# Optimization experiments

Hardware: AMD Instinct MI355X
Metric: run time of the kernel (lower is better)

## Reference

```python
import jax, jax.numpy as jnp
import numpy as np

# Hyperparameters (DetectionLoss __init__ defaults)
ALPHA = 0.75
GAMMA = 2.0
NUM_NEG = 10000
NUM_HARD = 100
NEG_POS_RATIO = 100
FN_WEIGHT = 4.0
FN_THRESHOLD = 0.8
HFP_T1 = 0.5
HFP_T2 = 0.7
HFP_W1 = 1.5
HFP_W2 = 2.0

B, N = 16, 884736  # batch, num anchor points (96^3 crop)


def setup_inputs() -> dict:
    key = jax.random.key(0)
    kp, kt, km = jax.random.split(key, 3)
    pred = jax.random.normal(kp, (B, N, 1), dtype=jnp.float32)
    # sparse binary positive targets (~440 positives per sample)
    target = (jax.random.uniform(kt, (B, N, 1)) < 5e-4).astype(jnp.float32)
    mask_ignore = (jax.random.uniform(km, (B, N, 1)) < 1e-2).astype(jnp.float32)
    mask_ignore = mask_ignore * (1.0 - target)
    return {"pred": pred, "target": target, "mask_ignore": mask_ignore}


def _bce_with_logits(x, t):
    # numerically stable binary_cross_entropy_with_logits, reduction='none'
    return jnp.maximum(x, 0.0) - x * t + jnp.log1p(jnp.exp(-jnp.abs(x)))


def _cls_loss(pred, target, mask_ignore):
    b = pred.shape[0]
    pred = pred.reshape(b, -1)
    target = target.reshape(b, -1)
    mask_ignore = mask_ignore.reshape(b, -1)
    # fixed keys replace python random.sample for negative subsampling
    keys = jax.random.split(jax.random.key(42), b)

    def per_sample(pred_b, target_b, mask_b, key):
        is_pos = target_b == 1.0
        is_neg = target_b == 0.0
        cls_prob = jnp.clip(jax.nn.sigmoid(jax.lax.stop_gradient(pred_b)), 1e-4, 1.0 - 1e-4)
        alpha_factor = jnp.where(is_pos, ALPHA, 1.0 - ALPHA)
        focal_w = alpha_factor * jnp.where(is_pos, 1.0 - cls_prob, cls_prob) ** GAMMA
        loss = jnp.where(mask_b == 0.0, focal_w * _bce_with_logits(pred_b, target_b), 0.0)
        npos = jnp.sum(is_pos)
        # false-negative upweight (only positive points qualify, so it is a
        # no-op in the npos==0 branch, matching the torch control flow)
        loss = loss * jnp.where((cls_prob < FN_THRESHOLD) & is_pos, FN_WEIGHT, 1.0)
        # hard false-positive upweight (applied in both branches)
        hfp_w = HFP_W1 + jnp.clip((cls_prob - HFP_T1) / (HFP_T2 - HFP_T1), 0.0, 1.0) * (HFP_W2 - HFP_W1)
        loss = loss * jnp.where((cls_prob > HFP_T1) & is_neg, hfp_w, 1.0)
        pos_loss = jnp.sum(jnp.where(is_pos, loss, 0.0))
        # random subsample of NUM_NEG negatives without replacement:
        # top-NUM_NEG by uniform random score restricted to negatives
        rnd = jax.random.uniform(key, pred_b.shape)
        sample_score = jnp.where(is_neg, rnd, -jnp.inf)
        _, idx = jax.lax.top_k(sample_score, NUM_NEG)
        neg_losses = jnp.where(is_neg[idx], loss[idx], 0.0)
        # hard-negative mining: keep top-k of the sampled negative losses
        topv = jax.lax.top_k(neg_losses, NUM_NEG)[0]
        k = jnp.where(npos > 0, jnp.minimum(NEG_POS_RATIO * npos, NUM_NEG), NUM_HARD)
        neg_sum = jnp.sum(jnp.where(jnp.arange(NUM_NEG) < k, topv, 0.0))
        # pos branch divides both sums by npos; neg branch divides by 1
        denom = jnp.where(npos > 0, jnp.maximum(npos.astype(pred_b.dtype), 1.0), 1.0)
        return pos_loss / denom, neg_sum / denom

    pos, neg = jax.vmap(per_sample)(pred, target, mask_ignore, keys)
    cls_pos_loss = jnp.sum(pos) / b
    cls_neg_loss = jnp.sum(neg) / b
    return jnp.stack([cls_pos_loss, cls_neg_loss])


def reference(pred, target, mask_ignore):
    return _cls_loss(pred, target, mask_ignore)
```

## Files before the change

### kernel.cpp

```cpp
#include <hip/hip_runtime.h>
#include <stdint.h>


#define BATCH 16
#define NPTS 884736u
#define THRESH_KEY 8266976u
#define THRESH_W   4232691712u
#define KEYMAX 8388607u
#define KSEL 10000u
#define TLO 8285746u
#define THI 8301746u
#define TLO_W 4242301952u
#define HI_W  4250494464u
#define WCAP 3072u
#define LCAP 64
#define SCAP 160
#define BCAP 64
#define NBLK 432u
#define EPT 8u
#define HDRB 512


struct KeyPairs { unsigned k[2 * BATCH]; };

__host__ __device__ __forceinline__ void tf2x32(unsigned k0, unsigned k1,
                                                unsigned x0, unsigned x1,
                                                unsigned& o0, unsigned& o1)
{
  unsigned ks0 = k0, ks1 = k1, ks2 = k0 ^ k1 ^ 0x1BD11BDAu;
  x0 += ks0; x1 += ks1;
#define TF_R(r) { x0 += x1; x1 = __builtin_rotateleft32(x1, r); x1 ^= x0; }
  TF_R(13) TF_R(15) TF_R(26) TF_R(6)
  x0 += ks1; x1 += ks2 + 1u;
  TF_R(17) TF_R(29) TF_R(16) TF_R(24)
  x0 += ks2; x1 += ks0 + 2u;
  TF_R(13) TF_R(15) TF_R(26) TF_R(6)
  x0 += ks0; x1 += ks1 + 3u;
  TF_R(17) TF_R(29) TF_R(16) TF_R(24)
  x0 += ks1; x1 += ks2 + 4u;
  TF_R(13) TF_R(15) TF_R(26) TF_R(6)
  x0 += ks2; x1 += ks0 + 5u;
#undef TF_R
  o0 = x0; o1 = x1;
}

__device__ __forceinline__ float lossf(float x, float t, float m)
{
  float e  = __expf(-x);
  float p  = __fdividef(1.0f, 1.0f + e);
  p = fminf(fmaxf(p, 1e-4f), 1.0f - 1e-4f);
  bool is_pos = (t == 1.0f);
  float alpha = is_pos ? 0.75f : 0.25f;
  float pw = is_pos ? (1.0f - p) : p;
  float soft = __logf(1.0f + __expf(-fabsf(x)));
  float bce = fmaxf(x, 0.0f) - x * t + soft;
  float L = (m == 0.0f) ? alpha * pw * pw * bce : 0.0f;
  if (is_pos && p < 0.8f) L *= 4.0f;
  if (!is_pos && p > 0.5f)
    L *= 1.5f + fminf(fmaxf((p - 0.5f) * 5.0f, 0.0f), 1.0f) * 0.5f;
  return L;
}

__global__ __launch_bounds__(256) void mono(
    const float* __restrict__ pred, const float* __restrict__ target,
    const float* __restrict__ mask, char* __restrict__ hdr,
    unsigned* __restrict__ wkey, unsigned* __restrict__ widx,
    float* __restrict__ wloss, KeyPairs kp)
{
  const int b = blockIdx.y;
  const int tid = threadIdx.x;
  const unsigned i0 = (blockIdx.x * 256u + tid) * EPT;
  const size_t sbase = (size_t)b * NPTS;
  const size_t off = sbase + i0;
  const unsigned k0 = kp.k[2 * b], k1 = kp.k[2 * b + 1];
  char* line = hdr + (size_t)b * HDRB;

  __shared__ unsigned s_n, s_wn, s_base, s_candhi, s_pos;
  __shared__ float    s_psum, s_hsum;
  __shared__ unsigned s_si[SCAP], s_skey[SCAP];
  __shared__ unsigned s_wk[LCAP], s_wi[LCAP];
  __shared__ float    s_wl[LCAP];

  if (tid == 0) {
    s_n = 0; s_wn = 0; s_candhi = 0; s_pos = 0;
    s_psum = 0.0f; s_hsum = 0.0f;
  }
  __syncthreads();

  float4 t4a = *reinterpret_cast<const float4*>(target + off);
  float4 t4b = *reinterpret_cast<const float4*>(target + off + 4);
  float tv[8] = { t4a.x, t4a.y, t4a.z, t4a.w, t4b.x, t4b.y, t4b.z, t4b.w };

  unsigned kw[8];
#pragma unroll
  for (int r = 0; r < 8; ++r) {
    unsigned o0, o1;
    tf2x32(k0, k1, 0u, i0 + (unsigned)r, o0, o1);
    kw[r] = o0 ^ o1;
  }

  unsigned candm = 0, posm = 0, him = 0, winm = 0;
#pragma unroll
  for (int r = 0; r < 8; ++r) {
    bool c  = (tv[r] == 0.0f) && (kw[r] >= THRESH_W);
    bool hi = c && (kw[r] >= HI_W);
    bool wn = c && !hi && (kw[r] >= TLO_W);
    candm |= (unsigned)c  << r;
    him   |= (unsigned)hi << r;
    winm  |= (unsigned)wn << r;
    posm  |= (unsigned)(tv[r] == 1.0f) << r;
  }

  if (candm) atomicAdd(&s_candhi, (unsigned)__popc(candm) | ((unsigned)__popc(him) << 16));
  if (posm)  atomicAdd(&s_pos, (unsigned)__popc(posm));

  const unsigned flags = him | winm | posm;
  if (flags) {
#pragma unroll
    for (int r = 0; r < 8; ++r) {
      if ((flags >> r) & 1u) {
        unsigned cls = ((posm >> r) & 1u) ? 2u : (((winm >> r) & 1u) ? 1u : 0u);
        unsigned p = atomicAdd(&s_n, 1u);
        if (p < SCAP) {
          s_si[p] = (i0 + (unsigned)r) | (cls << 20);
          s_skey[p] = kw[r] >> 9;
        } else {
          float x = pred[off + r], m = mask[off + r];
          float L = lossf(x, (cls == 2u) ? 1.0f : 0.0f, m);
          if (cls == 2u) atomicAdd(&s_psum, L);
          else if (cls == 0u) atomicAdd(&s_hsum, L);
          else {
            unsigned w = atomicAdd(&s_wn, 1u);
            if (w < LCAP) { s_wk[w] = kw[r] >> 9; s_wi[w] = i0 + (unsigned)r; s_wl[w] = L; }
          }
        }
      }
    }
  }
  __syncthreads();

  unsigned n = s_n < SCAP ? s_n : SCAP;
  for (unsigned e = tid; e < n; e += 256) {
    unsigned rec = s_si[e];
    unsigned i = rec & 0xFFFFFu, cls = rec >> 20;
    float x = pred[sbase + i], m = mask[sbase + i];
    float L = lossf(x, (cls == 2u) ? 1.0f : 0.0f, m);
    if (cls == 2u) atomicAdd(&s_psum, L);
    else if (cls == 0u) atomicAdd(&s_hsum, L);
    else {
      unsigned w = atomicAdd(&s_wn, 1u);
      if (w < LCAP) { s_wk[w] = s_skey[e]; s_wi[w] = i; s_wl[w] = L; }
    }
  }
  __syncthreads();

  if (tid == 0) {
    unsigned c = s_candhi & 0xFFFFu, h = s_candhi >> 16, p = s_pos;
    if (c) atomicAdd((unsigned*)(line + 64), c);
    if (h) { atomicAdd((unsigned*)(line + 128), h); atomicAdd((float*)(line + 132), s_hsum); }
    if (p) { atomicAdd((unsigned*)(line + 4), p); atomicAdd((float*)(line + 0), s_psum); }
    unsigned wn = s_wn;
    if (wn > LCAP) { atomicOr((unsigned*)(line + 196), 1u); wn = LCAP; }
    s_base = wn ? atomicAdd((unsigned*)(line + 192), wn) : 0u;
    s_wn = wn;
  }
  __syncthreads();
  unsigned wn = s_wn, gb = s_base;
  for (unsigned e = tid; e < wn; e += 256) {
    unsigned g = gb + e;
    if (g < WCAP) {
      wkey[b * WCAP + g] = s_wk[e];
      widx[b * WCAP + g] = s_wi[e];
      wloss[b * WCAP + g] = s_wl[e];
    }
  }
}

__global__ __launch_bounds__(256) void select_k(
    const float* __restrict__ pred, const float* __restrict__ target,
    const float* __restrict__ mask, char* __restrict__ hdr,
    const unsigned* __restrict__ wkey, const unsigned* __restrict__ widx,
    const float* __restrict__ wloss, float* __restrict__ out, KeyPairs kp)
{
  const int b = blockIdx.x;
  const int tid = threadIdx.x;
  char* line = hdr + (size_t)b * HDRB;
  unsigned* ticket = (unsigned*)(hdr + (size_t)BATCH * HDRB - 4);

  __shared__ unsigned skey[WCAP], sidx[WCAP];
  __shared__ float    sls[WCAP];
  __shared__ unsigned redu[256];
  __shared__ float    redf[256];
  __shared__ unsigned s_eqc, s_u1, s_tick;
  __shared__ unsigned s_eqi[BCAP];
  __shared__ float    s_eql[BCAP];
  __shared__ float    s_f;

  const unsigned cnt    = *(const unsigned*)(line + 64);
  const unsigned n_hi   = *(const unsigned*)(line + 128);
  const float    sum_hi = *(const float*)(line + 132);
  const unsigned n_win  = *(const unsigned*)(line + 192);
  const unsigned fail   = *(const unsigned*)(line + 196);
  const unsigned npos   = *(const unsigned*)(line + 4);
  const bool take_all = (cnt <= KSEL);
  const unsigned nsel = take_all ? cnt : KSEL;
  const unsigned k = (npos > 0u) ? ((100u * npos < KSEL) ? 100u * npos : KSEL) : 100u;
  const bool bad = fail || take_all || (n_hi > KSEL) ||
                   (n_hi + n_win < KSEL) || (n_win > WCAP) || (k < nsel);

  auto redSumU = [&](unsigned v) -> unsigned {
    redu[tid] = v; __syncthreads();
    for (int s = 128; s > 0; s >>= 1) { if (tid < s) redu[tid] += redu[tid + s]; __syncthreads(); }
    unsigned r = redu[0]; __syncthreads(); return r;
  };
  auto redSumF = [&](float v) -> float {
    redf[tid] = v; __syncthreads();
    for (int s = 128; s > 0; s >>= 1) { if (tid < s) redf[tid] += redf[tid + s]; __syncthreads(); }
    float r = redf[0]; __syncthreads(); return r;
  };

  float res = 0.0f;

  if (!bad) {
    const unsigned nw = n_win;
    for (unsigned e = tid; e < nw; e += 256) {
      skey[e] = wkey[b * WCAP + e];
      sidx[e] = widx[b * WCAP + e];
      sls[e]  = wloss[b * WCAP + e];
    }
    __syncthreads();
    const unsigned need = KSEL - n_hi;
    if (need == 0) res = sum_hi;
    else {
      auto cGe = [&](unsigned v) -> unsigned {
        unsigned c = 0;
        for (unsigned e = tid; e < nw; e += 256) c += (skey[e] >= v) ? 1u : 0u;
        return redSumU(c);
      };
      unsigned lo = TLO, hi = THI;
      while (lo < hi) {
        unsigned mid = lo + (hi - lo + 1u) / 2u;
        if (cGe(mid) >= need) lo = mid; else hi = mid - 1u;
      }
      const unsigned V = lo;
      const unsigned c_gt = cGe(V + 1u);
      const unsigned m = need - c_gt;
      float s = 0.0f;
      for (unsigned e = tid; e < nw; e += 256) if (skey[e] > V) s += sls[e];
      float sum_gt = redSumF(s);
      if (tid == 0) s_eqc = 0;
      __syncthreads();
      for (unsigned e = tid; e < nw; e += 256) {
        if (skey[e] == V) {
          unsigned p = atomicAdd(&s_eqc, 1u);
          if (p < BCAP) { s_eqi[p] = sidx[e]; s_eql[p] = sls[e]; }
        }
      }
      __syncthreads();
      if (tid == 0) {
        unsigned ne = s_eqc; if (ne > BCAP) ne = BCAP;
        unsigned mm = (m < ne) ? m : ne;
        float es = 0.0f;
        for (unsigned a = 0; a < mm; ++a) {
          unsigned best = a;
          for (unsigned q = a + 1; q < ne; ++q)
            if (s_eqi[q] < s_eqi[best]) best = q;
          unsigned ti = s_eqi[a]; s_eqi[a] = s_eqi[best]; s_eqi[best] = ti;
          float tl = s_eql[a]; s_eql[a] = s_eql[best]; s_eql[best] = tl;
          es += s_eql[a];
        }
        s_f = sum_hi + sum_gt + es;
      }
      __syncthreads();
      res = s_f;
    }
  } else {
    const float* T = target + (size_t)b * NPTS;
    const float* P = pred   + (size_t)b * NPTS;
    const float* M = mask   + (size_t)b * NPTS;
    const unsigned k0 = kp.k[2 * b], k1 = kp.k[2 * b + 1];
    auto keyOf = [&](unsigned i) -> unsigned {
      unsigned o0, o1; tf2x32(k0, k1, 0u, i, o0, o1); return (o0 ^ o1) >> 9;
    };
    auto cKeyGe = [&](unsigned v) -> unsigned {
      unsigned c = 0;
      for (unsigned i = tid; i < NPTS; i += 256)
        if (T[i] == 0.0f && keyOf(i) >= v) c++;
      return redSumU(c);
    };
    unsigned V = 0, idxcut = 0xffffffffu; float eq_sum = 0.0f;
    if (!take_all) {
      unsigned lo = THRESH_KEY, hi = KEYMAX;
      while (lo < hi) {
        unsigned mid = lo + (hi - lo + 1u) / 2u;
        if (cKeyGe(mid) >= KSEL) lo = mid; else hi = mid - 1u;
      }
      V = lo;
      unsigned c_gt = cKeyGe(V + 1u);
      unsigned needq = KSEL - c_gt;
      if (tid == 0) s_eqc = 0;
      __syncthreads();
      for (unsigned i = tid; i < NPTS; i += 256)
        if (T[i] == 0.0f && keyOf(i) == V) {
          unsigned p = atomicAdd(&s_eqc, 1u);
          if (p < BCAP) s_eqi[p] = i;
        }
      __syncthreads();
      if (tid == 0) {
        unsigned ne = s_eqc; if (ne > BCAP) ne = BCAP;
        unsigned mm = (needq < ne) ? needq : ne;
        float es = 0.0f; unsigned ic = 0xffffffffu;
        for (unsigned a = 0; a < mm; ++a) {
          unsigned best = a;
          for (unsigned q = a + 1; q < ne; ++q)
            if (s_eqi[q] < s_eqi[best]) best = q;
          unsigned ti = s_eqi[a]; s_eqi[a] = s_eqi[best]; s_eqi[best] = ti;
          es += lossf(P[s_eqi[a]], 0.0f, M[s_eqi[a]]);
        }
        if (mm > 0) ic = s_eqi[mm - 1];
        s_f = es; s_u1 = ic;
      }
      __syncthreads();
      eq_sum = s_f; idxcut = s_u1;
      __syncthreads();
    }
    if (k >= nsel) {
      float s = 0.0f;
      for (unsigned i = tid; i < NPTS; i += 256) {
        if (T[i] != 0.0f) continue;
        unsigned kk = keyOf(i);
        if (kk < THRESH_KEY) continue;
        if (take_all || kk > V) s += lossf(P[i], 0.0f, M[i]);
      }
      res = redSumF(s) + (take_all ? 0.0f : eq_sum);
    } else {
      auto cLossGe = [&](unsigned w) -> unsigned {
        unsigned c = 0;
        for (unsigned i = tid; i < NPTS; i += 256) {
          if (T[i] != 0.0f) continue;
          unsigned kk = keyOf(i);
          if (kk < THRESH_KEY) continue;
          bool sel = take_all || kk > V || (kk == V && i <= idxcut);
          if (sel && __float_as_uint(lossf(P[i], 0.0f, M[i])) >= w) c++;
        }
        return redSumU(c);
      };
      unsigned lo = 0u, hi = 0x7f7fffffu;
      while (lo < hi) {
        unsigned mid = lo + (hi - lo + 1u) / 2u;
        if (cLossGe(mid) >= k) lo = mid; else hi = mid - 1u;
      }
      unsigned cgt = cLossGe(lo + 1u);
      float s = 0.0f;
      for (unsigned i = tid; i < NPTS; i += 256) {
        if (T[i] != 0.0f) continue;
        unsigned kk = keyOf(i);
        if (kk < THRESH_KEY) continue;
        bool sel = take_all || kk > V || (kk == V && i <= idxcut);
        float L = lossf(P[i], 0.0f, M[i]);
        if (sel && __float_as_uint(L) > lo) s += L;
      }
      res = redSumF(s) + (float)(k - cgt) * __uint_as_float(lo);
    }
  }

  if (tid == 0) {
    atomicExch((float*)(line + 256), res);
    __threadfence();
    s_tick = atomicAdd(ticket, 1u);
  }
  __syncthreads();
  if (s_tick == BATCH - 1) {
    float ps = 0.0f, ns = 0.0f;
    if (tid < BATCH) {
      char* ln = hdr + (size_t)tid * HDRB;
      float pp = atomicAdd((float*)(ln + 0), 0.0f);
      unsigned np = atomicAdd((unsigned*)(ln + 4), 0u);
      float nr = atomicAdd((float*)(ln + 256), 0.0f);
      float denom = (np > 0u) ? fmaxf((float)np, 1.0f) : 1.0f;
      ps = pp / denom;
      ns = nr / denom;
    }
#pragma unroll
    for (int s = 8; s > 0; s >>= 1) {
      ps += __shfl_down(ps, s, 64);
      ns += __shfl_down(ns, s, 64);
    }
    if (tid == 0) {
      out[0] = ps / (float)BATCH;
      out[1] = ns / (float)BATCH;
    }
  }
}

extern "C" void kernel_launch(void* const* d_in, const int* in_sizes, int n_in,
                              void* d_out, int out_size, void* d_ws, size_t ws_size,
                              hipStream_t stream)
{
  const float* pred   = (const float*)d_in[0];
  const float* target = (const float*)d_in[1];
  const float* mask   = (const float*)d_in[2];
  float* out = (float*)d_out;

  const size_t HDRSZ = (size_t)BATCH * HDRB;
  const size_t FIXED = HDRSZ + 3 * (size_t)BATCH * WCAP * 4;
  if (ws_size < FIXED || out_size < 2) {
    hipMemsetAsync(d_out, 0, sizeof(float) * (out_size > 0 ? out_size : 1), stream);
    return;
  }

  char* ws = (char*)d_ws;
  char*     hdr   = ws;
  unsigned* wkey  = (unsigned*)(ws + HDRSZ);
  unsigned* widx  = wkey + (size_t)BATCH * WCAP;
  float*    wloss = (float*)(widx + (size_t)BATCH * WCAP);

  KeyPairs kp;
  for (unsigned b = 0; b < BATCH; ++b) {
    unsigned o0, o1;
    tf2x32(0u, 42u, 0u, b, o0, o1);
    kp.k[2 * b] = o0; kp.k[2 * b + 1] = o1;
  }

  hipMemsetAsync(hdr, 0, HDRSZ, stream);

  mono<<<dim3(NBLK, BATCH), 256, 0, stream>>>(pred, target, mask, hdr,
                                              wkey, widx, wloss, kp);
  select_k<<<BATCH, 256, 0, stream>>>(pred, target, mask, hdr,
                                      wkey, widx, wloss, out, kp);
}
```

Measured before the change: 85.06 us.

## Fuse selection into the main kernel via a per-sample last-block ticket

The separate select_k launch is removed. Each block of the streaming kernel takes a per-sample atomic ticket after writing its winners, and the last block of each sample runs the threshold selection and final reduction. To keep shared memory low, only keys are staged in LDS and index/loss values are re-read from global memory. This saves a kernel launch and its gap, but raises LDS use for every block of the big grid, which may reduce occupancy of the streaming phase.

```diff
diff --git a/kernel.cpp b/kernel.cpp
--- a/kernel.cpp
+++ b/kernel.cpp
@@ -61,11 +61,11 @@
   return L;
 }
 
-__global__ __launch_bounds__(256) void mono(
+__global__ __launch_bounds__(256) void fused(
     const float* __restrict__ pred, const float* __restrict__ target,
     const float* __restrict__ mask, char* __restrict__ hdr,
     unsigned* __restrict__ wkey, unsigned* __restrict__ widx,
-    float* __restrict__ wloss, KeyPairs kp)
+    float* __restrict__ wloss, float* __restrict__ out, KeyPairs kp)
 {
   const int b = blockIdx.y;
   const int tid = threadIdx.x;
@@ -74,12 +74,22 @@
   const size_t off = sbase + i0;
   const unsigned k0 = kp.k[2 * b], k1 = kp.k[2 * b + 1];
   char* line = hdr + (size_t)b * HDRB;
-
-  __shared__ unsigned s_n, s_wn, s_base, s_candhi, s_pos;
+  unsigned* gticket = (unsigned*)(hdr + (size_t)BATCH * HDRB - 4);
+
+  __shared__ unsigned s_n, s_wn, s_base, s_candhi, s_pos, s_tick;
   __shared__ float    s_psum, s_hsum;
   __shared__ unsigned s_si[SCAP], s_skey[SCAP];
   __shared__ unsigned s_wk[LCAP], s_wi[LCAP];
   __shared__ float    s_wl[LCAP];
+  __shared__ unsigned skey[WCAP];
+  __shared__ unsigned redu[256];
+  __shared__ float    redf[256];
+  __shared__ unsigned s_eqc, s_u1, s_fin;
+  __shared__ unsigned s_eqi[BCAP];
+  __shared__ float    s_eql[BCAP];
+  __shared__ float    s_f;
+  __shared__ unsigned h_cnt, h_nhi, h_nwin, h_fail, h_npos;
+  __shared__ float    h_sumhi;
 
   if (tid == 0) {
     s_n = 0; s_wn = 0; s_candhi = 0; s_pos = 0;
@@ -165,43 +175,37 @@
     s_wn = wn;
   }
   __syncthreads();
-  unsigned wn = s_wn, gb = s_base;
-  for (unsigned e = tid; e < wn; e += 256) {
-    unsigned g = gb + e;
-    if (g < WCAP) {
-      wkey[b * WCAP + g] = s_wk[e];
-      widx[b * WCAP + g] = s_wi[e];
-      wloss[b * WCAP + g] = s_wl[e];
-    }
-  }
-}
-
-__global__ __launch_bounds__(256) void select_k(
-    const float* __restrict__ pred, const float* __restrict__ target,
-    const float* __restrict__ mask, char* __restrict__ hdr,
-    const unsigned* __restrict__ wkey, const unsigned* __restrict__ widx,
-    const float* __restrict__ wloss, float* __restrict__ out, KeyPairs kp)
-{
-  const int b = blockIdx.x;
-  const int tid = threadIdx.x;
-  char* line = hdr + (size_t)b * HDRB;
-  unsigned* ticket = (unsigned*)(hdr + (size_t)BATCH * HDRB - 4);
-
-  __shared__ unsigned skey[WCAP], sidx[WCAP];
-  __shared__ float    sls[WCAP];
-  __shared__ unsigned redu[256];
-  __shared__ float    redf[256];
-  __shared__ unsigned s_eqc, s_u1, s_tick;
-  __shared__ unsigned s_eqi[BCAP];
-  __shared__ float    s_eql[BCAP];
-  __shared__ float    s_f;
-
-  const unsigned cnt    = *(const unsigned*)(line + 64);
-  const unsigned n_hi   = *(const unsigned*)(line + 128);
-  const float    sum_hi = *(const float*)(line + 132);
-  const unsigned n_win  = *(const unsigned*)(line + 192);
-  const unsigned fail   = *(const unsigned*)(line + 196);
-  const unsigned npos   = *(const unsigned*)(line + 4);
+  {
+    unsigned wn = s_wn, gb = s_base;
+    for (unsigned e = tid; e < wn; e += 256) {
+      unsigned g = gb + e;
+      if (g < WCAP) {
+        wkey[b * WCAP + g] = s_wk[e];
+        widx[b * WCAP + g] = s_wi[e];
+        wloss[b * WCAP + g] = s_wl[e];
+      }
+    }
+  }
+
+  if (tid == 0) {
+    __threadfence();
+    s_tick = atomicAdd((unsigned*)(line + 200), 1u);
+  }
+  __syncthreads();
+  if (s_tick != NBLK - 1) return;
+
+  if (tid == 0) {
+    h_cnt   = atomicAdd((unsigned*)(line + 64), 0u);
+    h_nhi   = atomicAdd((unsigned*)(line + 128), 0u);
+    h_sumhi = atomicAdd((float*)(line + 132), 0.0f);
+    h_nwin  = atomicAdd((unsigned*)(line + 192), 0u);
+    h_fail  = atomicAdd((unsigned*)(line + 196), 0u);
+    h_npos  = atomicAdd((unsigned*)(line + 4), 0u);
+  }
+  __syncthreads();
+  const unsigned cnt = h_cnt, n_hi = h_nhi, n_win = h_nwin, fail = h_fail,
+                 npos = h_npos;
+  const float sum_hi = h_sumhi;
   const bool take_all = (cnt <= KSEL);
   const unsigned nsel = take_all ? cnt : KSEL;
   const unsigned k = (npos > 0u) ? ((100u * npos < KSEL) ? 100u * npos : KSEL) : 100u;
@@ -223,11 +227,7 @@
 
   if (!bad) {
     const unsigned nw = n_win;
-    for (unsigned e = tid; e < nw; e += 256) {
-      skey[e] = wkey[b * WCAP + e];
-      sidx[e] = widx[b * WCAP + e];
-      sls[e]  = wloss[b * WCAP + e];
-    }
+    for (unsigned e = tid; e < nw; e += 256) skey[e] = wkey[b * WCAP + e];
     __syncthreads();
     const unsigned need = KSEL - n_hi;
     if (need == 0) res = sum_hi;
@@ -246,14 +246,15 @@
       const unsigned c_gt = cGe(V + 1u);
       const unsigned m = need - c_gt;
       float s = 0.0f;
-      for (unsigned e = tid; e < nw; e += 256) if (skey[e] > V) s += sls[e];
+      for (unsigned e = tid; e < nw; e += 256)
+        if (skey[e] > V) s += wloss[b * WCAP + e];
       float sum_gt = redSumF(s);
       if (tid == 0) s_eqc = 0;
       __syncthreads();
       for (unsigned e = tid; e < nw; e += 256) {
         if (skey[e] == V) {
           unsigned p = atomicAdd(&s_eqc, 1u);
-          if (p < BCAP) { s_eqi[p] = sidx[e]; s_eql[p] = sls[e]; }
+          if (p < BCAP) { s_eqi[p] = widx[b * WCAP + e]; s_eql[p] = wloss[b * WCAP + e]; }
         }
       }
       __syncthreads();
@@ -275,10 +276,9 @@
       res = s_f;
     }
   } else {
-    const float* T = target + (size_t)b * NPTS;
-    const float* P = pred   + (size_t)b * NPTS;
-    const float* M = mask   + (size_t)b * NPTS;
-    const unsigned k0 = kp.k[2 * b], k1 = kp.k[2 * b + 1];
+    const float* T = target + sbase;
+    const float* P = pred   + sbase;
+    const float* M = mask   + sbase;
     auto keyOf = [&](unsigned i) -> unsigned {
       unsigned o0, o1; tf2x32(k0, k1, 0u, i, o0, o1); return (o0 ^ o1) >> 9;
     };
@@ -367,10 +367,10 @@
   if (tid == 0) {
     atomicExch((float*)(line + 256), res);
     __threadfence();
-    s_tick = atomicAdd(ticket, 1u);
-  }
-  __syncthreads();
-  if (s_tick == BATCH - 1) {
+    s_fin = atomicAdd(gticket, 1u);
+  }
+  __syncthreads();
+  if (s_fin == BATCH - 1) {
     float ps = 0.0f, ns = 0.0f;
     if (tid < BATCH) {
       char* ln = hdr + (size_t)tid * HDRB;
@@ -424,8 +424,6 @@
 
   hipMemsetAsync(hdr, 0, HDRSZ, stream);
 
-  mono<<<dim3(NBLK, BATCH), 256, 0, stream>>>(pred, target, mask, hdr,
-                                              wkey, widx, wloss, kp);
-  select_k<<<BATCH, 256, 0, stream>>>(pred, target, mask, hdr,
-                                      wkey, widx, wloss, out, kp);
+  fused<<<dim3(NBLK, BATCH), 256, 0, stream>>>(pred, target, mask, hdr,
+                                               wkey, widx, wloss, out, kp);
 }
```

Result: slower. 257.5 us (+202.8%).

## Streamline per-block candidate compaction with batched atomics and wave-aggregated global writes

Applied to the files above, without the earlier changes.

The main kernel drops the total-candidate counter and the local window buffer. It reserves shared slots with one atomicAdd per thread instead of one per element, and writes window candidates directly to global memory using a wave ballot so only one global atomic is issued per wavefront. This removes a syncthreads phase and the extra per-block header atomics. The take_all count is now recomputed by a full scan only in the fallback path, and the fast path now requires k equal to KSEL.

```diff
diff --git a/kernel.cpp b/kernel.cpp
--- a/kernel.cpp
+++ b/kernel.cpp
@@ -13,7 +13,6 @@
 #define TLO_W 4242301952u
 #define HI_W  4250494464u
 #define WCAP 3072u
-#define LCAP 64
 #define SCAP 160
 #define BCAP 64
 #define NBLK 432u
@@ -75,16 +74,11 @@
   const unsigned k0 = kp.k[2 * b], k1 = kp.k[2 * b + 1];
   char* line = hdr + (size_t)b * HDRB;
 
-  __shared__ unsigned s_n, s_wn, s_base, s_candhi, s_pos;
+  __shared__ unsigned s_n, s_nhi, s_npos;
   __shared__ float    s_psum, s_hsum;
   __shared__ unsigned s_si[SCAP], s_skey[SCAP];
-  __shared__ unsigned s_wk[LCAP], s_wi[LCAP];
-  __shared__ float    s_wl[LCAP];
-
-  if (tid == 0) {
-    s_n = 0; s_wn = 0; s_candhi = 0; s_pos = 0;
-    s_psum = 0.0f; s_hsum = 0.0f;
-  }
+
+  if (tid == 0) { s_n = 0; s_nhi = 0; s_npos = 0; s_psum = 0.0f; s_hsum = 0.0f; }
   __syncthreads();
 
   float4 t4a = *reinterpret_cast<const float4*>(target + off);
@@ -99,39 +93,42 @@
     kw[r] = o0 ^ o1;
   }
 
-  unsigned candm = 0, posm = 0, him = 0, winm = 0;
+  unsigned posm = 0, him = 0, winm = 0;
 #pragma unroll
   for (int r = 0; r < 8; ++r) {
     bool c  = (tv[r] == 0.0f) && (kw[r] >= THRESH_W);
     bool hi = c && (kw[r] >= HI_W);
     bool wn = c && !hi && (kw[r] >= TLO_W);
-    candm |= (unsigned)c  << r;
     him   |= (unsigned)hi << r;
     winm  |= (unsigned)wn << r;
     posm  |= (unsigned)(tv[r] == 1.0f) << r;
   }
 
-  if (candm) atomicAdd(&s_candhi, (unsigned)__popc(candm) | ((unsigned)__popc(him) << 16));
-  if (posm)  atomicAdd(&s_pos, (unsigned)__popc(posm));
-
   const unsigned flags = him | winm | posm;
   if (flags) {
+    unsigned nf = (unsigned)__popc(flags);
+    unsigned base = atomicAdd(&s_n, nf);
+    unsigned j = 0;
 #pragma unroll
     for (int r = 0; r < 8; ++r) {
       if ((flags >> r) & 1u) {
         unsigned cls = ((posm >> r) & 1u) ? 2u : (((winm >> r) & 1u) ? 1u : 0u);
-        unsigned p = atomicAdd(&s_n, 1u);
+        unsigned p = base + j; ++j;
         if (p < SCAP) {
           s_si[p] = (i0 + (unsigned)r) | (cls << 20);
           s_skey[p] = kw[r] >> 9;
         } else {
           float x = pred[off + r], m = mask[off + r];
           float L = lossf(x, (cls == 2u) ? 1.0f : 0.0f, m);
-          if (cls == 2u) atomicAdd(&s_psum, L);
-          else if (cls == 0u) atomicAdd(&s_hsum, L);
+          if (cls == 2u) { atomicAdd(&s_psum, L); atomicAdd(&s_npos, 1u); }
+          else if (cls == 0u) { atomicAdd(&s_hsum, L); atomicAdd(&s_nhi, 1u); }
           else {
-            unsigned w = atomicAdd(&s_wn, 1u);
-            if (w < LCAP) { s_wk[w] = kw[r] >> 9; s_wi[w] = i0 + (unsigned)r; s_wl[w] = L; }
+            unsigned g = atomicAdd((unsigned*)(line + 192), 1u);
+            if (g < WCAP) {
+              wkey[b * WCAP + g] = kw[r] >> 9;
+              widx[b * WCAP + g] = i0 + (unsigned)r;
+              wloss[b * WCAP + g] = L;
+            } else atomicOr((unsigned*)(line + 196), 1u);
           }
         }
       }
@@ -139,40 +136,41 @@
   }
   __syncthreads();
 
-  unsigned n = s_n < SCAP ? s_n : SCAP;
-  for (unsigned e = tid; e < n; e += 256) {
-    unsigned rec = s_si[e];
-    unsigned i = rec & 0xFFFFFu, cls = rec >> 20;
+  const unsigned n = s_n < SCAP ? s_n : SCAP;
+  unsigned rec = (tid < (int)n) ? s_si[tid] : 0u;
+  unsigned cls = (tid < (int)n) ? (rec >> 20) : 3u;
+  unsigned i = rec & 0xFFFFFu;
+  float L = 0.0f;
+  if (cls < 3u) {
     float x = pred[sbase + i], m = mask[sbase + i];
-    float L = lossf(x, (cls == 2u) ? 1.0f : 0.0f, m);
-    if (cls == 2u) atomicAdd(&s_psum, L);
-    else if (cls == 0u) atomicAdd(&s_hsum, L);
-    else {
-      unsigned w = atomicAdd(&s_wn, 1u);
-      if (w < LCAP) { s_wk[w] = s_skey[e]; s_wi[w] = i; s_wl[w] = L; }
+    L = lossf(x, (cls == 2u) ? 1.0f : 0.0f, m);
+  }
+  if (cls == 2u) { atomicAdd(&s_psum, L); atomicAdd(&s_npos, 1u); }
+  else if (cls == 0u) { atomicAdd(&s_hsum, L); atomicAdd(&s_nhi, 1u); }
+  {
+    bool isw = (cls == 1u);
+    unsigned long long mv = __ballot(isw ? 1 : 0);
+    if (isw) {
+      int lane = tid & 63;
+      unsigned rank = (unsigned)__popcll(mv & ((1ull << lane) - 1ull));
+      int leader = __ffsll((unsigned long long)mv) - 1;
+      unsigned gb = 0;
+      if (lane == leader)
+        gb = atomicAdd((unsigned*)(line + 192), (unsigned)__popcll(mv));
+      gb = __shfl(gb, leader, 64);
+      unsigned g = gb + rank;
+      if (g < WCAP) {
+        wkey[b * WCAP + g] = s_skey[tid];
+        widx[b * WCAP + g] = i;
+        wloss[b * WCAP + g] = L;
+      } else atomicOr((unsigned*)(line + 196), 1u);
     }
   }
   __syncthreads();
 
   if (tid == 0) {
-    unsigned c = s_candhi & 0xFFFFu, h = s_candhi >> 16, p = s_pos;
-    if (c) atomicAdd((unsigned*)(line + 64), c);
-    if (h) { atomicAdd((unsigned*)(line + 128), h); atomicAdd((float*)(line + 132), s_hsum); }
-    if (p) { atomicAdd((unsigned*)(line + 4), p); atomicAdd((float*)(line + 0), s_psum); }
-    unsigned wn = s_wn;
-    if (wn > LCAP) { atomicOr((unsigned*)(line + 196), 1u); wn = LCAP; }
-    s_base = wn ? atomicAdd((unsigned*)(line + 192), wn) : 0u;
-    s_wn = wn;
-  }
-  __syncthreads();
-  unsigned wn = s_wn, gb = s_base;
-  for (unsigned e = tid; e < wn; e += 256) {
-    unsigned g = gb + e;
-    if (g < WCAP) {
-      wkey[b * WCAP + g] = s_wk[e];
-      widx[b * WCAP + g] = s_wi[e];
-      wloss[b * WCAP + g] = s_wl[e];
-    }
+    if (s_nhi) { atomicAdd((unsigned*)(line + 128), s_nhi); atomicAdd((float*)(line + 132), s_hsum); }
+    if (s_npos) { atomicAdd((unsigned*)(line + 4), s_npos); atomicAdd((float*)(line + 0), s_psum); }
   }
 }
 
@@ -185,7 +183,7 @@
   const int b = blockIdx.x;
   const int tid = threadIdx.x;
   char* line = hdr + (size_t)b * HDRB;
-  unsigned* ticket = (unsigned*)(hdr + (size_t)BATCH * HDRB - 4);
+  unsigned* gticket = (unsigned*)(hdr + (size_t)BATCH * HDRB - 4);
 
   __shared__ unsigned skey[WCAP], sidx[WCAP];
   __shared__ float    sls[WCAP];
@@ -196,17 +194,14 @@
   __shared__ float    s_eql[BCAP];
   __shared__ float    s_f;
 
-  const unsigned cnt    = *(const unsigned*)(line + 64);
   const unsigned n_hi   = *(const unsigned*)(line + 128);
   const float    sum_hi = *(const float*)(line + 132);
   const unsigned n_win  = *(const unsigned*)(line + 192);
   const unsigned fail   = *(const unsigned*)(line + 196);
   const unsigned npos   = *(const unsigned*)(line + 4);
-  const bool take_all = (cnt <= KSEL);
-  const unsigned nsel = take_all ? cnt : KSEL;
   const unsigned k = (npos > 0u) ? ((100u * npos < KSEL) ? 100u * npos : KSEL) : 100u;
-  const bool bad = fail || take_all || (n_hi > KSEL) ||
-                   (n_hi + n_win < KSEL) || (n_win > WCAP) || (k < nsel);
+  const bool bad = fail || (n_hi > KSEL) || (n_hi + n_win < KSEL) ||
+                   (n_win > WCAP) || (k < KSEL);
 
   auto redSumU = [&](unsigned v) -> unsigned {
     redu[tid] = v; __syncthreads();
@@ -288,6 +283,9 @@
         if (T[i] == 0.0f && keyOf(i) >= v) c++;
       return redSumU(c);
     };
+    const unsigned cnt = cKeyGe(THRESH_KEY);
+    const bool take_all = (cnt <= KSEL);
+    const unsigned nsel = take_all ? cnt : KSEL;
     unsigned V = 0, idxcut = 0xffffffffu; float eq_sum = 0.0f;
     if (!take_all) {
       unsigned lo = THRESH_KEY, hi = KEYMAX;
@@ -367,7 +365,7 @@
   if (tid == 0) {
     atomicExch((float*)(line + 256), res);
     __threadfence();
-    s_tick = atomicAdd(ticket, 1u);
+    s_tick = atomicAdd(gticket, 1u);
   }
   __syncthreads();
   if (s_tick == BATCH - 1) {
```

Measured after the change: 75.79 us. 1.12x faster.
